# Kernel optimization log

Measured on AMD Instinct MI355X. Metric: run time of the kernel, lower is better.

## Reference

```python
import jax, jax.numpy as jnp
import numpy as np

D_MODEL = 1024
NUM_HEADS = 16
D_HEAD = D_MODEL // NUM_HEADS
MAX_SEQ_LEN = 2048
THETA = 10000.0
BATCH = 2
SEQ = 2048


def _rope_tables():
    # inv_freq over even dims; emb interleaves each freq twice: [f0,f0,f1,f1,...]
    inv_freq = 1.0 / (THETA ** (jnp.arange(0, D_HEAD, 2, dtype=jnp.float32) / D_HEAD))
    t = jnp.arange(MAX_SEQ_LEN, dtype=jnp.float32)
    freqs = jnp.einsum('i,j->ij', t, inv_freq)  # [S, d_head/2]
    emb = jnp.stack((freqs, freqs), axis=-1).reshape(MAX_SEQ_LEN, D_HEAD)
    return jnp.cos(emb), jnp.sin(emb)


def _rotate_half(x):
    # pairwise interleaved rotation: (x0,x1,x2,x3,...) -> (-x1,x0,-x3,x2,...)
    xr = x.reshape(x.shape[:-1] + (D_HEAD // 2, 2))
    x1, x2 = xr[..., 0], xr[..., 1]
    return jnp.stack((-x2, x1), axis=-1).reshape(x.shape)


def setup_inputs() -> dict:
    key = jax.random.key(0)
    ks = jax.random.split(key, 5)
    std = np.sqrt(2.0 / (D_MODEL + D_MODEL)).astype(np.float32)
    return {
        'in_features': jax.random.normal(ks[0], (BATCH, SEQ, D_MODEL), dtype=jnp.float32),
        'token_positions': jnp.arange(SEQ, dtype=jnp.int64) if jax.config.jax_enable_x64 else jnp.arange(SEQ, dtype=jnp.int32),
        'wq': jax.random.normal(ks[1], (D_MODEL, D_MODEL), dtype=jnp.float32) * std,
        'wk': jax.random.normal(ks[2], (D_MODEL, D_MODEL), dtype=jnp.float32) * std,
        'wv': jax.random.normal(ks[3], (D_MODEL, D_MODEL), dtype=jnp.float32) * std,
        'wo': jax.random.normal(ks[4], (D_MODEL, D_MODEL), dtype=jnp.float32) * std,
    }


def reference(in_features, token_positions, wq, wk, wv, wo):
    b, s, _ = in_features.shape
    cos_tab, sin_tab = _rope_tables()
    cos = cos_tab[token_positions]  # [s, d_head]
    sin = sin_tab[token_positions]

    def split_heads(t):  # [b, s, d_model] -> [b, h, s, d_head]
        return t.reshape(b, s, NUM_HEADS, D_HEAD).transpose(0, 2, 1, 3)

    q = split_heads(jnp.einsum('bsd,ed->bse', in_features, wq))
    k = split_heads(jnp.einsum('bsd,ed->bse', in_features, wk))
    v = split_heads(jnp.einsum('bsd,ed->bse', in_features, wv))

    q = q * cos + _rotate_half(q) * sin
    k = k * cos + _rotate_half(k) * sin

    scale = 1.0 / np.sqrt(D_HEAD).astype(np.float32)
    scores = jnp.einsum('bhqd,bhkd->bhqk', q, k) * scale  # [b,h,s,s]
    causal = jnp.tril(jnp.ones((s, s), dtype=bool))
    scores = jnp.where(causal, scores, -jnp.inf)
    weights = jax.nn.softmax(scores, axis=-1)
    out = jnp.einsum('bhqk,bhkd->bhqd', weights, v)
    out = out.transpose(0, 2, 1, 3).reshape(b, s, D_MODEL)
    return jnp.einsum('bsd,ed->bse', out, wo)
```

## Files before the change

### kernel.cpp

```cpp
#include <hip/hip_runtime.h>


typedef __attribute__((ext_vector_type(8))) short bf16x8;
typedef __attribute__((ext_vector_type(4))) float f32x4;

__device__ __forceinline__ short f2bf(float f) {
  unsigned u = __float_as_uint(f);
  unsigned r = (u + 0x7fffu + ((u >> 16) & 1u)) >> 16;
  return (short)(r & 0xFFFFu);
}

__device__ __forceinline__ unsigned pk2(float a, float b) {
  return __builtin_amdgcn_perm(__float_as_uint(b) + 0x8000u,
                               __float_as_uint(a) + 0x8000u, 0x07060302u);
}

__device__ __forceinline__ void async16(const void* g, void* l) {
  __builtin_amdgcn_global_load_lds(
      (const __attribute__((address_space(1))) void*)g,
      (__attribute__((address_space(3))) void*)l, 16, 0, 0);
}

__device__ __forceinline__ void cstore(short* C, size_t i, float v) { C[i] = f2bf(v); }
__device__ __forceinline__ void cstore(float* C, size_t i, float v) { C[i] = v; }

__global__ void cast_all(const float4* __restrict__ X,
                         const float4* __restrict__ w0, const float4* __restrict__ w1,
                         const float4* __restrict__ w2, const float4* __restrict__ w3,
                         short* __restrict__ Xb, short* __restrict__ Wb) {
  int t = blockIdx.x * 256 + threadIdx.x;
  const float4* s;
  short4* d;
  if (t < (1 << 20)) {
    s = X + t; d = (short4*)Xb + t;
  } else {
    int u = t - (1 << 20);
    int which = u >> 18;
    s = ((which == 0) ? w0 : (which == 1) ? w1 : (which == 2) ? w2 : w3) + (u & 0x3FFFF);
    d = (short4*)Wb + u;
  }
  float4 v = *s;
  *d = make_short4(f2bf(v.x), f2bf(v.y), f2bf(v.z), f2bf(v.w));
}

enum EpiMode { EPI_ROW, EPI_KFRAG, EPI_VFRAG };

template <typename OUT, int MR, int NR, bool ROPE, EpiMode EM>
__device__ __forceinline__ void gemm_core(short* __restrict__ As, short* __restrict__ Bs,
                                          const short* __restrict__ A, const short* __restrict__ B,
                                          OUT* __restrict__ C, int bm, int bn, int ldc,
                                          const int* __restrict__ pos) {
  constexpr int BM = 32 * MR, BN = 32 * NR;
  constexpr int NLD = (BM * 4 + BN * 4) / 256;
  const int tid  = threadIdx.x;
  const int lane = tid & 63, wave = tid >> 6;
  const int col  = lane & 15, quad = lane >> 4;
  const int wm = (wave & 1) * (16 * MR), wn = (wave >> 1) * (16 * NR);

  f32x4 acc[MR][NR];
#pragma unroll
  for (int i = 0; i < MR; i++)
#pragma unroll
    for (int j = 0; j < NR; j++) acc[i][j] = (f32x4){0.f, 0.f, 0.f, 0.f};

  auto stage = [&](int k0, int bu) {
#pragma unroll
    for (int c = tid; c < BM * 4; c += 256) {
      int r = c >> 2, cc = (c & 3) << 3;
      async16(A + (size_t)(bm + r) * 1024 + k0 + cc, As + bu * BM * 32 + c * 8);
    }
#pragma unroll
    for (int c = tid; c < BN * 4; c += 256) {
      int r = c >> 2, cc = (c & 3) << 3;
      async16(B + (size_t)(bn + r) * 1024 + k0 + cc, Bs + bu * BN * 32 + c * 8);
    }
  };

  stage(0, 0);
  stage(32, 1);
  if constexpr (NLD == 4) asm volatile("s_waitcnt vmcnt(4)" ::: "memory");
  else                    asm volatile("s_waitcnt vmcnt(3)" ::: "memory");
  __builtin_amdgcn_s_barrier();

  int cur = 0, nxt = 2;
  for (int it = 0; it < 32; ++it) {
    if (it < 30) stage((it + 2) * 32, nxt);
    const short* as = As + cur * (BM * 32);
    const short* bs = Bs + cur * (BN * 32);

    bf16x8 af[MR], bfr[NR];
#pragma unroll
    for (int i = 0; i < MR; i++)
      af[i] = *(const bf16x8*)(as + (wm + i * 16 + col) * 32 + quad * 8);
#pragma unroll
    for (int i = 0; i < NR; i++)
      bfr[i] = *(const bf16x8*)(bs + (wn + i * 16 + col) * 32 + quad * 8);
#pragma unroll
    for (int mi = 0; mi < MR; mi++)
#pragma unroll
      for (int ni = 0; ni < NR; ni++)
        acc[mi][ni] = __builtin_amdgcn_mfma_f32_16x16x32_bf16(af[mi], bfr[ni], acc[mi][ni], 0, 0, 0);

    if (it < 30) {
      if constexpr (NLD == 4) asm volatile("s_waitcnt vmcnt(4)" ::: "memory");
      else                    asm volatile("s_waitcnt vmcnt(3)" ::: "memory");
    } else {
      asm volatile("s_waitcnt vmcnt(0)" ::: "memory");
    }
    __builtin_amdgcn_s_barrier();
    cur = (cur == 2) ? 0 : cur + 1;
    nxt = (nxt == 2) ? 0 : nxt + 1;
  }

  if (ROPE) {
    float invf_rev[NR];
#pragma unroll
    for (int ni = 0; ni < NR; ni++) {
      int pr = ((bn + wn + ni * 16 + col) & 63) >> 1;
      invf_rev[ni] = exp2f(-0.4152410118609203f * (float)pr) * 0.15915494309189535f;
    }
    const float sgn = (col & 1) ? 1.f : -1.f;
#pragma unroll
    for (int mi = 0; mi < MR; mi++) {
#pragma unroll
      for (int r = 0; r < 4; r++) {
        int row = bm + wm + mi * 16 + quad * 4 + r;
        float fp = (float)pos[row & 2047];
#pragma unroll
        for (int ni = 0; ni < NR; ni++) {
          float rev = fp * invf_rev[ni];
          rev -= floorf(rev);
          float sn = __builtin_amdgcn_sinf(rev);
          float cs = __builtin_amdgcn_cosf(rev);
          float x  = acc[mi][ni][r];
          float px = __shfl_xor(x, 1);
          acc[mi][ni][r] = fmaf(x, cs, sgn * px * sn);
        }
      }
    }
  }

  if (EM == EPI_ROW) {
#pragma unroll
    for (int mi = 0; mi < MR; mi++) {
#pragma unroll
      for (int r = 0; r < 4; r++) {
        size_t row = (size_t)(bm + wm + mi * 16 + quad * 4 + r);
#pragma unroll
        for (int ni = 0; ni < NR; ni++) {
          int cg = bn + wn + ni * 16 + col;
          cstore(C, row * ldc + cg, acc[mi][ni][r]);
        }
      }
    }
  } else if (EM == EPI_KFRAG) {
#pragma unroll
    for (int mi = 0; mi < MR; mi++) {
#pragma unroll
      for (int r = 0; r < 4; r++) {
        int m = bm + wm + mi * 16 + quad * 4 + r;
        int bq = m >> 11, key = m & 2047;
        int kt = key >> 6, nb = (key >> 4) & 3, cl = key & 15;
#pragma unroll
        for (int ni = 0; ni < NR; ni++) {
          int e = bn + wn + ni * 16 + col;
          int h = e >> 6, d = e & 63;
          size_t seg = ((((size_t)(bq * 16 + h) * 32 + kt) * 4 + nb) * 2 + (d >> 5));
          cstore((short*)C, seg * 512 + (((d >> 3) & 3) * 16 + cl) * 8 + (d & 7), acc[mi][ni][r]);
        }
      }
    }
  } else {
#pragma unroll
    for (int mi = 0; mi < MR; mi++) {
#pragma unroll
      for (int r = 0; r < 4; r++) {
        int e = bm + wm + mi * 16 + quad * 4 + r;
        int h = e >> 6, d = e & 63;
        int nb = d >> 4, cl = d & 15;
#pragma unroll
        for (int ni = 0; ni < NR; ni++) {
          int m = bn + wn + ni * 16 + col;
          int bq = m >> 11, key = m & 2047;
          int kt = key >> 6, k64 = key & 63;
          size_t seg = ((((size_t)(bq * 16 + h) * 32 + kt) * 4 + nb) * 2 + (k64 >> 5));
          cstore((short*)C, seg * 512 + (((k64 >> 3) & 3) * 16 + cl) * 8 + (k64 & 7), acc[mi][ni][r]);
        }
      }
    }
  }
}

__global__ __launch_bounds__(256, 3) void qkv_gemm(const short* __restrict__ Xb,
                                                   const short* __restrict__ Wq,
                                                   const short* __restrict__ Wk,
                                                   const short* __restrict__ Wv,
                                                   short* __restrict__ Qo,
                                                   short* __restrict__ Kf,
                                                   short* __restrict__ Vf,
                                                   const int* __restrict__ pos) {
  __shared__ __align__(16) short sm[3 * 128 * 32 + 3 * 128 * 32];
  short* As = sm;
  short* Bs = sm + 3 * 128 * 32;
  const int z = blockIdx.z;
  if (z == 0)      gemm_core<short, 4, 4, true,  EPI_ROW  >(As, Bs, Xb, Wq, Qo, blockIdx.x * 128, blockIdx.y * 128, 1024, pos);
  else if (z == 1) gemm_core<short, 4, 4, true,  EPI_KFRAG>(As, Bs, Xb, Wk, Kf, blockIdx.x * 128, blockIdx.y * 128, 0, pos);
  else             gemm_core<short, 4, 4, false, EPI_VFRAG>(As, Bs, Wv, Xb, Vf, blockIdx.y * 128, blockIdx.x * 128, 0, pos);
}

__global__ __launch_bounds__(256) void out_gemm(const short* __restrict__ Ctx,
                                                const short* __restrict__ Wo,
                                                float* __restrict__ C) {
  __shared__ __align__(16) short sm[3 * 64 * 32 + 3 * 128 * 32];
  gemm_core<float, 2, 4, false, EPI_ROW>(sm, sm + 3 * 64 * 32, Ctx, Wo, C,
                                         blockIdx.x * 64, blockIdx.y * 128, 1024, nullptr);
}

__global__ __launch_bounds__(256, 4) void flash_attn(const short* __restrict__ Q,
                                                     const short* __restrict__ Kf,
                                                     const short* __restrict__ Vf,
                                                     short* __restrict__ ctx) {
  const int y = blockIdx.y;
  const int g = y >> 3, r8 = y & 7;
  const int qt = (g == 0) ? 31 - r8 : (g == 1) ? r8 : (g == 2) ? 23 - r8 : 8 + r8;
  const int bh = blockIdx.x;
  const int b = bh >> 4, h = bh & 15;
  __shared__ __align__(16) short Ps[4][16 * 72];
  const int tid = threadIdx.x, lane = tid & 63, wave = tid >> 6;
  const int col = lane & 15, quad = lane >> 4;

  const short* Kfb = Kf + (size_t)bh * 131072 + lane * 8;
  const short* Vfb = Vf + (size_t)bh * 131072 + lane * 8;

  const float C1 = 0.18033688011112042f;
  const float C2 = 17.31234049066756f;

  short* myPs = &Ps[wave][0];
  const int cx = col & 3;
  const int pswr0 = col * 72 + ((0 ^ cx) << 4) + quad * 4;
  const int pswr1 = col * 72 + ((1 ^ cx) << 4) + quad * 4;
  const int pswr2 = col * 72 + ((2 ^ cx) << 4) + quad * 4;
  const int pswr3 = col * 72 + ((3 ^ cx) << 4) + quad * 4;
  const int psrd0 = col * 72 + (((quad >> 1) ^ cx) << 4) + (quad & 1) * 8;
  const int psrd1 = col * 72 + ((((quad >> 1) + 2) ^ cx) << 4) + (quad & 1) * 8;

  auto ldk = [&](int kt, bf16x8 (&kf)[4][2]) {
    const int base = kt * 4096;
#pragma unroll
    for (int nb = 0; nb < 4; nb++) {
      kf[nb][0] = *(const bf16x8*)(Kfb + base + (nb * 2 + 0) * 512);
      kf[nb][1] = *(const bf16x8*)(Kfb + base + (nb * 2 + 1) * 512);
    }
  };
  auto ldv = [&](int kt, bf16x8 (&vf)[4][2]) {
    const int base = kt * 4096;
#pragma unroll
    for (int nb = 0; nb < 4; nb++) {
      vf[nb][0] = *(const bf16x8*)(Vfb + base + (nb * 2 + 0) * 512);
      vf[nb][1] = *(const bf16x8*)(Vfb + base + (nb * 2 + 1) * 512);
    }
  };

  const size_t qrow = (size_t)(b * 2048 + qt * 64 + wave * 16 + col);
  bf16x8 qf0 = *(const bf16x8*)(Q + qrow * 1024 + h * 64 + quad * 8);
  bf16x8 qf1 = *(const bf16x8*)(Q + qrow * 1024 + h * 64 + 32 + quad * 8);

  float l_i = 0.f;
  f32x4 o_acc[4];
#pragma unroll
  for (int i = 0; i < 4; i++) o_acc[i] = (f32x4){0.f, 0.f, 0.f, 0.f};

  const int qg = qt * 64 + wave * 16 + col;
  bf16x8 kf[4][2], vf[4][2];
  ldk(0, kf);

  for (int kt = 0; kt <= qt; ++kt) {
    ldv(kt, vf);
    f32x4 s_acc[4];
#pragma unroll
    for (int nb = 0; nb < 4; nb++) {
      f32x4 z = (f32x4){0.f, 0.f, 0.f, 0.f};
      z = __builtin_amdgcn_mfma_f32_16x16x32_bf16(kf[nb][0], qf0, z, 0, 0, 0);
      z = __builtin_amdgcn_mfma_f32_16x16x32_bf16(kf[nb][1], qf1, z, 0, 0, 0);
      s_acc[nb] = z;
    }
    if (kt < qt) ldk(kt + 1, kf);
    const bool diag = (kt == qt);
#pragma unroll
    for (int nb = 0; nb < 4; nb++) {
      float pv[4];
#pragma unroll
      for (int r = 0; r < 4; r++) {
        pv[r] = exp2f(s_acc[nb][r] * C1 - C2);
        if (diag && (kt * 64 + nb * 16 + quad * 4 + r) > qg) pv[r] = 0.f;
        l_i += pv[r];
      }
      int wr = (nb == 0) ? pswr0 : (nb == 1) ? pswr1 : (nb == 2) ? pswr2 : pswr3;
      *(uint2*)(myPs + wr) = make_uint2(pk2(pv[0], pv[1]), pk2(pv[2], pv[3]));
    }
    bf16x8 af0 = *(const bf16x8*)(myPs + psrd0);
    bf16x8 af1 = *(const bf16x8*)(myPs + psrd1);
#pragma unroll
    for (int nb = 0; nb < 4; nb++) {
      o_acc[nb] = __builtin_amdgcn_mfma_f32_16x16x32_bf16(af0, vf[nb][0], o_acc[nb], 0, 0, 0);
      o_acc[nb] = __builtin_amdgcn_mfma_f32_16x16x32_bf16(af1, vf[nb][1], o_acc[nb], 0, 0, 0);
    }
  }

  l_i += __shfl_xor(l_i, 16);
  l_i += __shfl_xor(l_i, 32);
  float invl = 1.0f / l_i;

#pragma unroll
  for (int r = 0; r < 4; r++) {
    float inv = __shfl(invl, quad * 4 + r);
    size_t row = (size_t)(b * 2048 + qt * 64 + wave * 16 + quad * 4 + r);
#pragma unroll
    for (int nb = 0; nb < 4; nb++)
      ctx[row * 1024 + h * 64 + nb * 16 + col] = f2bf(o_acc[nb][r] * inv);
  }
}

extern "C" void kernel_launch(void* const* d_in, const int* in_sizes, int n_in,
                              void* d_out, int out_size, void* d_ws, size_t ws_size,
                              hipStream_t stream) {
  const float* X  = (const float*)d_in[0];
  const int* pos  = (const int*)d_in[1];
  const float* wq = (const float*)d_in[2];
  const float* wk = (const float*)d_in[3];
  const float* wv = (const float*)d_in[4];
  const float* wo = (const float*)d_in[5];
  float* out = (float*)d_out;

  short* Xb  = (short*)d_ws;
  short* Wqb = Xb + (1 << 22);
  short* Wkb = Wqb + (1 << 20);
  short* Wvb = Wkb + (1 << 20);
  short* Wob = Wvb + (1 << 20);
  short* Qb  = Wob + (1 << 20);
  short* Kfb = Qb + (1 << 22);
  short* Vfb = Kfb + (1 << 22);
  short* Ctx = Vfb + (1 << 22);

  cast_all<<<8192, 256, 0, stream>>>((const float4*)X, (const float4*)wq, (const float4*)wk,
                                     (const float4*)wv, (const float4*)wo, Xb, Wqb);
  qkv_gemm<<<dim3(32, 8, 3), 256, 0, stream>>>(Xb, Wqb, Wkb, Wvb, Qb, Kfb, Vfb, pos);
  flash_attn<<<dim3(32, 32), 256, 0, stream>>>(Qb, Kfb, Vfb, Ctx);
  out_gemm<<<dim3(64, 8), 256, 0, stream>>>(Ctx, Wob, out);
}
```

Measured before the change: 173.1 us.

## Stage K/V tiles in LDS with double-buffered async loads in flash attention

Replaces the per-wave direct global loads of K and V fragments with block-cooperative asynchronous global-to-LDS copies into double buffers. All four waves then read the shared tile from LDS, so each K/V tile is fetched from global memory once per block instead of once per wave. The cost is a block-wide barrier and vmcnt wait every iteration, more shared memory, and a lower occupancy hint (launch bounds from 4 to 3 blocks per CU).

```diff
diff --git a/kernel.cpp b/kernel.cpp
--- a/kernel.cpp
+++ b/kernel.cpp
@@ -216,7 +216,7 @@
                                          blockIdx.x * 64, blockIdx.y * 128, 1024, nullptr);
 }
 
-__global__ __launch_bounds__(256, 4) void flash_attn(const short* __restrict__ Q,
+__global__ __launch_bounds__(256, 3) void flash_attn(const short* __restrict__ Q,
                                                      const short* __restrict__ Kf,
                                                      const short* __restrict__ Vf,
                                                      short* __restrict__ ctx) {
@@ -226,11 +226,13 @@
   const int bh = blockIdx.x;
   const int b = bh >> 4, h = bh & 15;
   __shared__ __align__(16) short Ps[4][16 * 72];
+  __shared__ __align__(16) short Ksm[2][4096];
+  __shared__ __align__(16) short Vsm[2][4096];
   const int tid = threadIdx.x, lane = tid & 63, wave = tid >> 6;
   const int col = lane & 15, quad = lane >> 4;
 
-  const short* Kfb = Kf + (size_t)bh * 131072 + lane * 8;
-  const short* Vfb = Vf + (size_t)bh * 131072 + lane * 8;
+  const short* Kg = Kf + (size_t)bh * 131072;
+  const short* Vg = Vf + (size_t)bh * 131072;
 
   const float C1 = 0.18033688011112042f;
   const float C2 = 17.31234049066756f;
@@ -244,20 +246,13 @@
   const int psrd0 = col * 72 + (((quad >> 1) ^ cx) << 4) + (quad & 1) * 8;
   const int psrd1 = col * 72 + ((((quad >> 1) + 2) ^ cx) << 4) + (quad & 1) * 8;
 
-  auto ldk = [&](int kt, bf16x8 (&kf)[4][2]) {
-    const int base = kt * 4096;
-#pragma unroll
-    for (int nb = 0; nb < 4; nb++) {
-      kf[nb][0] = *(const bf16x8*)(Kfb + base + (nb * 2 + 0) * 512);
-      kf[nb][1] = *(const bf16x8*)(Kfb + base + (nb * 2 + 1) * 512);
-    }
-  };
-  auto ldv = [&](int kt, bf16x8 (&vf)[4][2]) {
-    const int base = kt * 4096;
-#pragma unroll
-    for (int nb = 0; nb < 4; nb++) {
-      vf[nb][0] = *(const bf16x8*)(Vfb + base + (nb * 2 + 0) * 512);
-      vf[nb][1] = *(const bf16x8*)(Vfb + base + (nb * 2 + 1) * 512);
+  auto stageKV = [&](int kt, int bu) {
+    const short* kg = Kg + kt * 4096;
+    const short* vg = Vg + kt * 4096;
+#pragma unroll
+    for (int c = tid; c < 512; c += 256) {
+      async16(kg + c * 8, &Ksm[bu][c * 8]);
+      async16(vg + c * 8, &Vsm[bu][c * 8]);
     }
   };
 
@@ -271,20 +266,33 @@
   for (int i = 0; i < 4; i++) o_acc[i] = (f32x4){0.f, 0.f, 0.f, 0.f};
 
   const int qg = qt * 64 + wave * 16 + col;
-  bf16x8 kf[4][2], vf[4][2];
-  ldk(0, kf);
+
+  stageKV(0, 0);
+  asm volatile("s_waitcnt vmcnt(0)" ::: "memory");
+  __builtin_amdgcn_s_barrier();
 
   for (int kt = 0; kt <= qt; ++kt) {
-    ldv(kt, vf);
+    const int cur = kt & 1;
+    if (kt < qt) stageKV(kt + 1, cur ^ 1);
+
+    bf16x8 kfr[4][2], vfr[4][2];
+#pragma unroll
+    for (int nb = 0; nb < 4; nb++) {
+      kfr[nb][0] = *(const bf16x8*)(&Ksm[cur][(nb * 2 + 0) * 512] + lane * 8);
+      kfr[nb][1] = *(const bf16x8*)(&Ksm[cur][(nb * 2 + 1) * 512] + lane * 8);
+      vfr[nb][0] = *(const bf16x8*)(&Vsm[cur][(nb * 2 + 0) * 512] + lane * 8);
+      vfr[nb][1] = *(const bf16x8*)(&Vsm[cur][(nb * 2 + 1) * 512] + lane * 8);
+    }
+
     f32x4 s_acc[4];
 #pragma unroll
     for (int nb = 0; nb < 4; nb++) {
       f32x4 z = (f32x4){0.f, 0.f, 0.f, 0.f};
-      z = __builtin_amdgcn_mfma_f32_16x16x32_bf16(kf[nb][0], qf0, z, 0, 0, 0);
-      z = __builtin_amdgcn_mfma_f32_16x16x32_bf16(kf[nb][1], qf1, z, 0, 0, 0);
+      z = __builtin_amdgcn_mfma_f32_16x16x32_bf16(kfr[nb][0], qf0, z, 0, 0, 0);
+      z = __builtin_amdgcn_mfma_f32_16x16x32_bf16(kfr[nb][1], qf1, z, 0, 0, 0);
       s_acc[nb] = z;
     }
-    if (kt < qt) ldk(kt + 1, kf);
+
     const bool diag = (kt == qt);
 #pragma unroll
     for (int nb = 0; nb < 4; nb++) {
@@ -302,8 +310,13 @@
     bf16x8 af1 = *(const bf16x8*)(myPs + psrd1);
 #pragma unroll
     for (int nb = 0; nb < 4; nb++) {
-      o_acc[nb] = __builtin_amdgcn_mfma_f32_16x16x32_bf16(af0, vf[nb][0], o_acc[nb], 0, 0, 0);
-      o_acc[nb] = __builtin_amdgcn_mfma_f32_16x16x32_bf16(af1, vf[nb][1], o_acc[nb], 0, 0, 0);
+      o_acc[nb] = __builtin_amdgcn_mfma_f32_16x16x32_bf16(af0, vfr[nb][0], o_acc[nb], 0, 0, 0);
+      o_acc[nb] = __builtin_amdgcn_mfma_f32_16x16x32_bf16(af1, vfr[nb][1], o_acc[nb], 0, 0, 0);
+    }
+
+    if (kt < qt) {
+      asm volatile("s_waitcnt vmcnt(0)" ::: "memory");
+      __builtin_amdgcn_s_barrier();
     }
   }
 
```

New measurement: 172.7 us. Within noise of the previous version (-0.2%).
